# Kernel optimization log

Measured on AMD Instinct MI355X. Metric: run time of the kernel, lower is better.

Reference implementation:

```python
import math
import jax, jax.numpy as jnp
import numpy as np

H, D_H = 16, 128  # heads, head_dim; d = H*D_H = 2048

def _heads_view(w, rank):
    # w: (d, r) -> (H, r, d_h), matching torch view(H, d_h, r).transpose(1, 2)
    return jnp.transpose(w.reshape(H, D_H, rank), (0, 2, 1))

def setup_inputs() -> dict:
    key = jax.random.key(0)
    ks = jax.random.split(key, 9)
    d, rq, rk, rv = 2048, 512, 512, 512
    B, T = 2, 2048
    s = 0.02  # GPT-2 style init scale keeps logits numerically sane
    return {
        "x": jax.random.normal(ks[0], (B, T, d), dtype=jnp.float32),
        "q_down_w": jax.random.normal(ks[1], (rq, d), dtype=jnp.float32) * s,
        "k_down_w": jax.random.normal(ks[2], (rk, d), dtype=jnp.float32) * s,
        "v_down_w": jax.random.normal(ks[3], (rv, d), dtype=jnp.float32) * s,
        "q_up_w": jax.random.normal(ks[4], (d, rq), dtype=jnp.float32) * s,
        "k_up_w": jax.random.normal(ks[5], (d, rk), dtype=jnp.float32) * s,
        "v_up_w": jax.random.normal(ks[6], (d, rv), dtype=jnp.float32) * s,
        "out_w": jax.random.normal(ks[7], (d, d), dtype=jnp.float32) * s,
        "out_b": jnp.zeros((d,), dtype=jnp.float32),
    }

def reference(x, q_down_w, k_down_w, v_down_w, q_up_w, k_up_w, v_up_w, out_w, out_b):
    B, T, d = x.shape
    rq, rk, rv = q_down_w.shape[0], k_down_w.shape[0], v_down_w.shape[0]
    # Down projections (nn.Linear: x @ W^T)
    Qd = x @ q_down_w.T            # [B, T, rq]
    Kd = x @ k_down_w.T            # [B, S, rk] (S == T, no past_kv)
    Vd = x @ v_down_w.T            # [B, S, rv]
    S = Kd.shape[1]
    # Absorbed score matrix M: [H, rq, rk]
    Uq_h = _heads_view(q_up_w, rq)  # [H, rq, d_h]
    Uk_h = _heads_view(k_up_w, rk)  # [H, rk, d_h]
    M = jnp.einsum('hqd,hkd->hqk', Uq_h, Uk_h) * (1.0 / math.sqrt(D_H))
    # Logits via factorized path: [B,H,T,rk] then [B,H,T,S]
    Qm = jnp.einsum('btq,hqk->bhtk', Qd, M)
    logits = jnp.einsum('bhtk,bsk->bhts', Qm, Kd)
    # Causal mask (P = S - T = 0)
    P = S - T
    i = jnp.arange(T)[:, None]
    j = jnp.arange(S)[None, :]
    future = j > (P + i)
    logits = jnp.where(future[None, None], -jnp.inf, logits)
    attn = jax.nn.softmax(logits.astype(jnp.float32), axis=-1)
    attn = jnp.nan_to_num(attn).astype(x.dtype)
    # Values path
    Uv_h = _heads_view(v_up_w, rv)                      # [H, rv, d_h]
    V_up = jnp.einsum('bsr,hrd->bhsd', Vd, Uv_h)        # [B, H, S, d_h]
    ctx = jnp.einsum('bhts,bhsd->bhtd', attn, V_up)     # [B, H, T, d_h]
    ctx = jnp.transpose(ctx, (0, 2, 1, 3)).reshape(B, T, d)
    out = ctx @ out_w.T + out_b
    return out
```

## Files before the change

kernel.cpp:

```cpp
#include <hip/hip_runtime.h>
#include <stdint.h>

typedef __bf16 bf16x8 __attribute__((ext_vector_type(8)));
typedef float  f32x4  __attribute__((ext_vector_type(4)));
typedef unsigned short u16;
typedef u16 u16x8 __attribute__((ext_vector_type(8)));

__device__ __forceinline__ u16 f2bf(float f) {
  uint32_t u = __builtin_bit_cast(uint32_t, f);
  u += 0x7fffu + ((u >> 16) & 1u);
  return (u16)(u >> 16);
}

__device__ __forceinline__ void async_cp16(const void* src, void* lds) {
  __builtin_amdgcn_global_load_lds(
      (const __attribute__((address_space(1))) uint32_t*)src,
      (__attribute__((address_space(3))) uint32_t*)lds, 16, 0, 0);
}

struct CvtArgs {
  const float* in[8];
  u16* out[8];
  int n8[8];
  int nblk[8];
};
__global__ void cvt_multi(CvtArgs a) {
  int bx = blockIdx.x;
  int t = 0;
  while (t < 7 && bx >= a.nblk[t]) { bx -= a.nblk[t]; ++t; }
  const int i = bx * 256 + threadIdx.x;
  if (i >= a.n8[t]) return;
  const float4* p = (const float4*)a.in[t] + (size_t)i * 2;
  float4 va = p[0], vb = p[1];
  u16x8 r;
  r[0] = f2bf(va.x); r[1] = f2bf(va.y); r[2] = f2bf(va.z); r[3] = f2bf(va.w);
  r[4] = f2bf(vb.x); r[5] = f2bf(vb.y); r[6] = f2bf(vb.z); r[7] = f2bf(vb.w);
  ((u16x8*)a.out[t])[i] = r;
}

struct GemmB3 {
  const u16* A[3];
  const u16* Bm[3];
  u16* C[3];
  float alpha[3];
};

template<bool F32OUT>
__global__ __launch_bounds__(256, 2)
void gemm_bt(GemmB3 args, float* __restrict__ Cf, const float* __restrict__ bias,
             int M, int N, int K)
{
  __shared__ u16 At[128 * 32];
  __shared__ u16 Bt[128 * 32];
  const int z = blockIdx.z;
  const u16* __restrict__ A  = args.A[z];
  const u16* __restrict__ Bw = args.Bm[z];
  const int bm = blockIdx.x * 128;
  const int bn = blockIdx.y * 128;
  const int tid = threadIdx.x;
  const int w  = tid >> 6;
  const int l  = tid & 63;
  const int lr = l & 15;
  const int lg = l >> 4;
  const int wr = (w >> 1) * 64;
  const int wc = (w & 1) * 64;

  f32x4 acc[4][4];
  #pragma unroll
  for (int m = 0; m < 4; ++m) {
    #pragma unroll
    for (int n = 0; n < 4; ++n) acc[m][n] = (f32x4){0.f, 0.f, 0.f, 0.f};
  }

  for (int k0 = 0; k0 < K; k0 += 32) {
    __syncthreads();
    #pragma unroll
    for (int i = 0; i < 2; ++i) {
      const int gidx = i * 256 + tid;
      const int row  = gidx >> 2;
      const int g    = gidx & 3;
      const int gs   = (g - (row >> 1)) & 3;
      async_cp16(A  + (size_t)(bm + row) * K + k0 + gs * 8,
                 At + (size_t)(i * 256 + w * 64) * 8);
      async_cp16(Bw + (size_t)(bn + row) * K + k0 + gs * 8,
                 Bt + (size_t)(i * 256 + w * 64) * 8);
    }
    __syncthreads();
    bf16x8 af[4], bfr[4];
    #pragma unroll
    for (int m = 0; m < 4; ++m) {
      const int row = wr + m * 16 + lr;
      const int pos = (lg + (row >> 1)) & 3;
      af[m] = *(const bf16x8*)(At + row * 32 + pos * 8);
    }
    #pragma unroll
    for (int n = 0; n < 4; ++n) {
      const int row = wc + n * 16 + lr;
      const int pos = (lg + (row >> 1)) & 3;
      bfr[n] = *(const bf16x8*)(Bt + row * 32 + pos * 8);
    }
    #pragma unroll
    for (int m = 0; m < 4; ++m) {
      #pragma unroll
      for (int n = 0; n < 4; ++n)
        acc[m][n] = __builtin_amdgcn_mfma_f32_16x16x32_bf16(af[m], bfr[n], acc[m][n], 0, 0, 0);
    }
  }

  if constexpr (F32OUT) {
    #pragma unroll
    for (int n = 0; n < 4; ++n) {
      const int col = bn + wc + n * 16 + lr;
      const float bv = bias[col];
      #pragma unroll
      for (int m = 0; m < 4; ++m) {
        const int rbase = bm + wr + m * 16 + lg * 4;
        #pragma unroll
        for (int j = 0; j < 4; ++j)
          Cf[(size_t)(rbase + j) * N + col] = acc[m][n][j] + bv;
      }
    }
  } else {
    u16* __restrict__ C = args.C[z];
    const float alpha = args.alpha[z];
    #pragma unroll
    for (int n = 0; n < 4; ++n) {
      const int col = bn + wc + n * 16 + lr;
      #pragma unroll
      for (int m = 0; m < 4; ++m) {
        const int rbase = bm + wr + m * 16 + lg * 4;
        #pragma unroll
        for (int j = 0; j < 4; ++j)
          C[(size_t)(rbase + j) * N + col] = f2bf(acc[m][n][j] * alpha);
      }
    }
  }
}

__global__ __launch_bounds__(256, 2)
void mla_attn(const u16* __restrict__ Qu, const u16* __restrict__ Ku,
              const u16* __restrict__ Vtg, u16* __restrict__ ctx)
{
  __shared__ u16 Ktb[2][64 * 128];
  __shared__ u16 Vtb[2][128 * 64];
  __shared__ u16 Pb[4][16 * 72];

  const int bid = blockIdx.x;
  const int kk  = bid >> 5;
  const int qt  = (kk & 1) ? (kk >> 1) : (31 - (kk >> 1));
  const int bh  = bid & 31;
  const int b = bh >> 4, h = bh & 15;
  const int qbase = qt * 64;
  const int tid = threadIdx.x;
  const int w = tid >> 6, l = tid & 63, lr = l & 15, lg = l >> 4;
  const int T = 2048;
  const size_t rs = 2048;
  const u16* Qp = Qu + ((size_t)b * T) * rs + (size_t)h * 128;
  const u16* Kp = Ku + ((size_t)b * T) * rs + (size_t)h * 128;
  const u16* Vp = Vtg + (size_t)(h * 128) * 4096 + (size_t)b * T;

  bf16x8 qf[4];
  const int qrow = qbase + w * 16 + lr;
  #pragma unroll
  for (int f = 0; f < 4; ++f)
    qf[f] = *(const bf16x8*)(Qp + (size_t)qrow * rs + f * 32 + lg * 8);

  f32x4 acc[8];
  #pragma unroll
  for (int f = 0; f < 8; ++f) acc[f] = (f32x4){0.f, 0.f, 0.f, 0.f};
  f32x4 lacc = (f32x4){0.f, 0.f, 0.f, 0.f};
  float mrun[4];
  #pragma unroll
  for (int j = 0; j < 4; ++j) mrun[j] = -INFINITY;

  u16x8 onebits;
  #pragma unroll
  for (int e = 0; e < 8; ++e) onebits[e] = 0x3F80;
  const bf16x8 ones = __builtin_bit_cast(bf16x8, onebits);

  u16* Pw = Pb[w];
  const int nT = qt + 1;

  auto stage = [&](int buf, int it) {
    const int s0 = it * 64;
    #pragma unroll
    for (int i = 0; i < 4; ++i) {
      const int gidx = i * 256 + tid;
      const int s = gidx >> 4, g = gidx & 15;
      async_cp16(Kp + (size_t)(s0 + s) * rs + ((g ^ (s & 7)) * 8),
                 &Ktb[buf][(i * 256 + w * 64) * 8]);
    }
    #pragma unroll
    for (int i = 0; i < 4; ++i) {
      const int gidx = i * 256 + tid;
      const int dh = gidx >> 3, g = gidx & 7;
      async_cp16(Vp + (size_t)dh * 4096 + s0 + ((g ^ (dh & 7)) * 8),
                 &Vtb[buf][(i * 256 + w * 64) * 8]);
    }
  };

  stage(0, 0);
  int cur = 0;

  for (int it = 0; it < nT; ++it) {
    __syncthreads();
    if (it + 1 < nT) stage(cur ^ 1, it + 1);
    const u16* Kt = Ktb[cur];
    const u16* Vt = Vtb[cur];

    f32x4 c[4];
    #pragma unroll
    for (int ct = 0; ct < 4; ++ct) c[ct] = (f32x4){0.f, 0.f, 0.f, 0.f};
    __builtin_amdgcn_s_setprio(1);
    #pragma unroll
    for (int ct = 0; ct < 4; ++ct) {
      const int row = ct * 16 + lr;
      #pragma unroll
      for (int f = 0; f < 4; ++f) {
        bf16x8 kf = *(const bf16x8*)(Kt + row * 128 + (((f * 4 + lg) ^ (lr & 7)) * 8));
        c[ct] = __builtin_amdgcn_mfma_f32_16x16x32_bf16(qf[f], kf, c[ct], 0, 0, 0);
      }
    }
    __builtin_amdgcn_s_setprio(0);

    float p[4][4], mx[4];
    if (it == nT - 1) {
      const int qg = qbase + w * 16 + lg * 4;
      #pragma unroll
      for (int j = 0; j < 4; ++j) mx[j] = -INFINITY;
      #pragma unroll
      for (int ct = 0; ct < 4; ++ct) {
        const int s = it * 64 + ct * 16 + lr;
        #pragma unroll
        for (int j = 0; j < 4; ++j) {
          p[ct][j] = (s <= qg + j) ? c[ct][j] : -INFINITY;
          mx[j] = fmaxf(mx[j], p[ct][j]);
        }
      }
    } else {
      #pragma unroll
      for (int ct = 0; ct < 4; ++ct)
        #pragma unroll
        for (int j = 0; j < 4; ++j) p[ct][j] = c[ct][j];
      #pragma unroll
      for (int j = 0; j < 4; ++j)
        mx[j] = fmaxf(fmaxf(p[0][j], p[1][j]), fmaxf(p[2][j], p[3][j]));
    }
    #pragma unroll
    for (int j = 0; j < 4; ++j) {
      #pragma unroll
      for (int off = 1; off < 16; off <<= 1)
        mx[j] = fmaxf(mx[j], __shfl_xor(mx[j], off));
    }
    int over = 0;
    #pragma unroll
    for (int j = 0; j < 4; ++j) over |= (mx[j] > mrun[j] + 8.f) ? 1 : 0;
    if (__any(over)) {
      #pragma unroll
      for (int j = 0; j < 4; ++j) {
        const float mnew = fmaxf(mrun[j], mx[j]);
        const float scl = exp2f(mrun[j] - mnew);
        mrun[j] = mnew;
        lacc[j] *= scl;
        #pragma unroll
        for (int f = 0; f < 8; ++f) acc[f][j] *= scl;
      }
    }
    #pragma unroll
    for (int ct = 0; ct < 4; ++ct)
      #pragma unroll
      for (int j = 0; j < 4; ++j) p[ct][j] = exp2f(p[ct][j] - mrun[j]);

    #pragma unroll
    for (int ct = 0; ct < 4; ++ct)
      #pragma unroll
      for (int j = 0; j < 4; ++j)
        Pw[(lg * 4 + j) * 72 + ct * 16 + lr] = f2bf(p[ct][j]);
    asm volatile("s_waitcnt lgkmcnt(0)" ::: "memory");
    __builtin_amdgcn_sched_barrier(0);
    bf16x8 pf0 = *(const bf16x8*)(Pw + lr * 72 + lg * 8);
    bf16x8 pf1 = *(const bf16x8*)(Pw + lr * 72 + 32 + lg * 8);

    __builtin_amdgcn_s_setprio(1);
    lacc = __builtin_amdgcn_mfma_f32_16x16x32_bf16(pf0, ones, lacc, 0, 0, 0);
    lacc = __builtin_amdgcn_mfma_f32_16x16x32_bf16(pf1, ones, lacc, 0, 0, 0);
    #pragma unroll
    for (int f = 0; f < 8; ++f) {
      const int row = f * 16 + lr;
      bf16x8 v0 = *(const bf16x8*)(Vt + row * 64 + ((lg ^ (lr & 7)) * 8));
      bf16x8 v1 = *(const bf16x8*)(Vt + row * 64 + (((4 + lg) ^ (lr & 7)) * 8));
      acc[f] = __builtin_amdgcn_mfma_f32_16x16x32_bf16(pf0, v0, acc[f], 0, 0, 0);
      acc[f] = __builtin_amdgcn_mfma_f32_16x16x32_bf16(pf1, v1, acc[f], 0, 0, 0);
    }
    __builtin_amdgcn_s_setprio(0);
    cur ^= 1;
  }

  __syncthreads();
  u16* Ot = &Ktb[0][0];
  float inv[4];
  #pragma unroll
  for (int j = 0; j < 4; ++j) inv[j] = 1.f / lacc[j];
  #pragma unroll
  for (int f = 0; f < 8; ++f) {
    #pragma unroll
    for (int j = 0; j < 4; ++j) {
      const int q = w * 16 + lg * 4 + j;
      const int dh = f * 16 + lr;
      Ot[q * 128 + (dh ^ ((q & 7) << 3))] = f2bf(acc[f][j] * inv[j]);
    }
  }
  __syncthreads();
  const size_t obase = ((size_t)b * T + qbase) * rs + (size_t)h * 128;
  #pragma unroll
  for (int i = 0; i < 4; ++i) {
    const int gi = i * 256 + tid;
    const int q = gi >> 4, g = gi & 15;
    bf16x8 v = *(const bf16x8*)(Ot + q * 128 + ((g ^ (q & 7)) * 8));
    *(bf16x8*)(ctx + obase + (size_t)q * rs + g * 8) = v;
  }
}

extern "C" void kernel_launch(void* const* d_in, const int* in_sizes, int n_in,
                              void* d_out, int out_size, void* d_ws, size_t ws_size,
                              hipStream_t stream)
{
  (void)n_in; (void)out_size; (void)ws_size;
  const float* x   = (const float*)d_in[0];
  const float* qdw = (const float*)d_in[1];
  const float* kdw = (const float*)d_in[2];
  const float* vdw = (const float*)d_in[3];
  const float* quw = (const float*)d_in[4];
  const float* kuw = (const float*)d_in[5];
  const float* vuw = (const float*)d_in[6];
  const float* oww = (const float*)d_in[7];
  const float* ob  = (const float*)d_in[8];

  const int d = 2048, r = 512;
  const int BT = in_sizes[0] / d;

  u16* p = (u16*)d_ws;
  auto take = [&](size_t n) { u16* q = p; p += n; return q; };
  u16* xb  = take((size_t)BT * d);
  u16* wqd = take((size_t)r * d);
  u16* wkd = take((size_t)r * d);
  u16* wvd = take((size_t)r * d);
  u16* wqu = take((size_t)d * r);
  u16* wku = take((size_t)d * r);
  u16* wvu = take((size_t)d * r);
  u16* wow = take((size_t)d * d);
  u16* Qd  = take((size_t)BT * r);
  u16* Kd  = take((size_t)BT * r);
  u16* Vd  = take((size_t)BT * r);
  u16* Qu  = take((size_t)BT * d);
  u16* Ku  = take((size_t)BT * d);
  u16* Vtg = take((size_t)BT * d);
  u16* ctx = take((size_t)BT * d);

  CvtArgs ca;
  const float* ins[8] = {x, oww, qdw, kdw, vdw, quw, kuw, vuw};
  u16* outs[8]        = {xb, wow, wqd, wkd, wvd, wqu, wku, wvu};
  const size_t ns[8]  = {(size_t)BT * d, (size_t)d * d,
                         (size_t)r * d, (size_t)r * d, (size_t)r * d,
                         (size_t)d * r, (size_t)d * r, (size_t)d * r};
  int total_blk = 0;
  for (int t = 0; t < 8; ++t) {
    ca.in[t] = ins[t]; ca.out[t] = outs[t];
    ca.n8[t] = (int)(ns[t] / 8);
    ca.nblk[t] = (ca.n8[t] + 255) / 256;
    total_blk += ca.nblk[t];
  }
  cvt_multi<<<dim3(total_blk), dim3(256), 0, stream>>>(ca);

  GemmB3 g1;
  g1.A[0] = xb;  g1.A[1] = xb;  g1.A[2] = xb;
  g1.Bm[0] = wqd; g1.Bm[1] = wkd; g1.Bm[2] = wvd;
  g1.C[0] = Qd;  g1.C[1] = Kd;  g1.C[2] = Vd;
  g1.alpha[0] = 1.f; g1.alpha[1] = 1.f; g1.alpha[2] = 1.f;
  gemm_bt<false><<<dim3(BT / 128, r / 128, 3), dim3(256), 0, stream>>>(
      g1, nullptr, nullptr, BT, r, d);

  GemmB3 g2;
  g2.A[0] = Qd;  g2.A[1] = Kd;  g2.A[2] = Kd;
  g2.Bm[0] = wqu; g2.Bm[1] = wku; g2.Bm[2] = wku;
  g2.C[0] = Qu;  g2.C[1] = Ku;  g2.C[2] = Ku;
  g2.alpha[0] = 0.12751743f; g2.alpha[1] = 1.f; g2.alpha[2] = 1.f;
  gemm_bt<false><<<dim3(BT / 128, d / 128, 2), dim3(256), 0, stream>>>(
      g2, nullptr, nullptr, BT, d, r);

  GemmB3 g2v;
  g2v.A[0] = wvu; g2v.A[1] = wvu; g2v.A[2] = wvu;
  g2v.Bm[0] = Vd; g2v.Bm[1] = Vd; g2v.Bm[2] = Vd;
  g2v.C[0] = Vtg; g2v.C[1] = Vtg; g2v.C[2] = Vtg;
  g2v.alpha[0] = 1.f; g2v.alpha[1] = 1.f; g2v.alpha[2] = 1.f;
  gemm_bt<false><<<dim3(d / 128, BT / 128, 1), dim3(256), 0, stream>>>(
      g2v, nullptr, nullptr, d, BT, r);

  mla_attn<<<dim3(1024), dim3(256), 0, stream>>>(Qu, Ku, Vtg, ctx);

  GemmB3 g3;
  g3.A[0] = ctx; g3.A[1] = ctx; g3.A[2] = ctx;
  g3.Bm[0] = wow; g3.Bm[1] = wow; g3.Bm[2] = wow;
  g3.C[0] = nullptr; g3.C[1] = nullptr; g3.C[2] = nullptr;
  g3.alpha[0] = 1.f; g3.alpha[1] = 1.f; g3.alpha[2] = 1.f;
  gemm_bt<true><<<dim3(BT / 128, d / 128, 1), dim3(256), 0, stream>>>(
      g3, (float*)d_out, ob, BT, d, d);
}
```

Measured before the change: 242.5 us.

## Rewrite attention kernel with 32x32 MFMA, 128-row query tiles and register P exchange

The flash attention kernel now uses 32x32x16 bf16 MFMAs, computing S^T so each lane owns one query row. Each block covers 128 query rows (32 per wave) instead of 64, so half as many blocks are launched and each K/V tile staged in shared memory is reused by more queries. The P matrix is rebuilt for the PV MFMA through lane shuffles instead of a round trip through shared memory, and row sums are accumulated in registers instead of by an MFMA against a ones vector. Waves whose rows lie entirely before a K tile skip it under the causal mask. The costs are higher register pressure from the 16-wide accumulators, half as many blocks for load balancing, and a new swizzle whose correctness depends on matching index math.

```diff
diff --git a/kernel.cpp b/kernel.cpp
--- a/kernel.cpp
+++ b/kernel.cpp
@@ -3,13 +3,19 @@
 
 typedef __bf16 bf16x8 __attribute__((ext_vector_type(8)));
 typedef float  f32x4  __attribute__((ext_vector_type(4)));
+typedef float  f32x16 __attribute__((ext_vector_type(16)));
 typedef unsigned short u16;
+typedef unsigned int u32;
 typedef u16 u16x8 __attribute__((ext_vector_type(8)));
+typedef u32 u32x4 __attribute__((ext_vector_type(4)));
 
 __device__ __forceinline__ u16 f2bf(float f) {
   uint32_t u = __builtin_bit_cast(uint32_t, f);
   u += 0x7fffu + ((u >> 16) & 1u);
   return (u16)(u >> 16);
+}
+__device__ __forceinline__ u32 pack2(float lo, float hi) {
+  return (u32)f2bf(lo) | ((u32)f2bf(hi) << 16);
 }
 
 __device__ __forceinline__ void async_cp16(const void* src, void* lds) {
@@ -67,10 +73,9 @@
 
   f32x4 acc[4][4];
   #pragma unroll
-  for (int m = 0; m < 4; ++m) {
+  for (int m = 0; m < 4; ++m)
     #pragma unroll
     for (int n = 0; n < 4; ++n) acc[m][n] = (f32x4){0.f, 0.f, 0.f, 0.f};
-  }
 
   for (int k0 = 0; k0 < K; k0 += 32) {
     __syncthreads();
@@ -100,11 +105,10 @@
       bfr[n] = *(const bf16x8*)(Bt + row * 32 + pos * 8);
     }
     #pragma unroll
-    for (int m = 0; m < 4; ++m) {
+    for (int m = 0; m < 4; ++m)
       #pragma unroll
       for (int n = 0; n < 4; ++n)
         acc[m][n] = __builtin_amdgcn_mfma_f32_16x16x32_bf16(af[m], bfr[n], acc[m][n], 0, 0, 0);
-    }
   }
 
   if constexpr (F32OUT) {
@@ -143,60 +147,55 @@
 {
   __shared__ u16 Ktb[2][64 * 128];
   __shared__ u16 Vtb[2][128 * 64];
-  __shared__ u16 Pb[4][16 * 72];
 
   const int bid = blockIdx.x;
   const int kk  = bid >> 5;
-  const int qt  = (kk & 1) ? (kk >> 1) : (31 - (kk >> 1));
+  const int qt  = (kk & 1) ? (kk >> 1) : (15 - (kk >> 1));
   const int bh  = bid & 31;
   const int b = bh >> 4, h = bh & 15;
-  const int qbase = qt * 64;
+  const int qbase = qt * 128;
   const int tid = threadIdx.x;
-  const int w = tid >> 6, l = tid & 63, lr = l & 15, lg = l >> 4;
+  const int w = tid >> 6, l = tid & 63;
+  const int ql = l & 31;
+  const int hi = l >> 5;
+  const bool hb = (hi != 0);
   const int T = 2048;
   const size_t rs = 2048;
+
   const u16* Qp = Qu + ((size_t)b * T) * rs + (size_t)h * 128;
   const u16* Kp = Ku + ((size_t)b * T) * rs + (size_t)h * 128;
   const u16* Vp = Vtg + (size_t)(h * 128) * 4096 + (size_t)b * T;
 
-  bf16x8 qf[4];
-  const int qrow = qbase + w * 16 + lr;
-  #pragma unroll
-  for (int f = 0; f < 4; ++f)
-    qf[f] = *(const bf16x8*)(Qp + (size_t)qrow * rs + f * 32 + lg * 8);
-
-  f32x4 acc[8];
-  #pragma unroll
-  for (int f = 0; f < 8; ++f) acc[f] = (f32x4){0.f, 0.f, 0.f, 0.f};
-  f32x4 lacc = (f32x4){0.f, 0.f, 0.f, 0.f};
-  float mrun[4];
-  #pragma unroll
-  for (int j = 0; j < 4; ++j) mrun[j] = -INFINITY;
-
-  u16x8 onebits;
-  #pragma unroll
-  for (int e = 0; e < 8; ++e) onebits[e] = 0x3F80;
-  const bf16x8 ones = __builtin_bit_cast(bf16x8, onebits);
-
-  u16* Pw = Pb[w];
-  const int nT = qt + 1;
+  const int qw = qbase + w * 32;
+  const int qg = qw + ql;
+
+  bf16x8 qf[8];
+  #pragma unroll
+  for (int kb = 0; kb < 8; ++kb)
+    qf[kb] = *(const bf16x8*)(Qp + (size_t)qg * rs + kb * 16 + hi * 8);
+
+  f32x16 acc[4];
+  #pragma unroll
+  for (int dt = 0; dt < 4; ++dt)
+    #pragma unroll
+    for (int r = 0; r < 16; ++r) acc[dt][r] = 0.f;
+  float mrun = -1.0e30f, lsum = 0.f;
+
+  const int ksr = tid >> 4;
+  const u16* kb0 = Kp + (size_t)ksr * rs + (((tid & 15) ^ (ksr & 15)) * 8);
+  const int vsr = tid >> 3;
+  const u16* vb0 = Vp + (size_t)vsr * 4096 + (((tid & 7) ^ (vsr & 7)) * 8);
+
+  const int nT = 2 * qt + 2;
 
   auto stage = [&](int buf, int it) {
     const int s0 = it * 64;
     #pragma unroll
-    for (int i = 0; i < 4; ++i) {
-      const int gidx = i * 256 + tid;
-      const int s = gidx >> 4, g = gidx & 15;
-      async_cp16(Kp + (size_t)(s0 + s) * rs + ((g ^ (s & 7)) * 8),
-                 &Ktb[buf][(i * 256 + w * 64) * 8]);
-    }
-    #pragma unroll
-    for (int i = 0; i < 4; ++i) {
-      const int gidx = i * 256 + tid;
-      const int dh = gidx >> 3, g = gidx & 7;
-      async_cp16(Vp + (size_t)dh * 4096 + s0 + ((g ^ (dh & 7)) * 8),
-                 &Vtb[buf][(i * 256 + w * 64) * 8]);
-    }
+    for (int i = 0; i < 4; ++i)
+      async_cp16(kb0 + (size_t)(s0 + i * 16) * rs, &Ktb[buf][(i * 256 + w * 64) * 8]);
+    #pragma unroll
+    for (int i = 0; i < 4; ++i)
+      async_cp16(vb0 + (size_t)(i * 32) * 4096 + s0, &Vtb[buf][(i * 256 + w * 64) * 8]);
   };
 
   stage(0, 0);
@@ -205,119 +204,110 @@
   for (int it = 0; it < nT; ++it) {
     __syncthreads();
     if (it + 1 < nT) stage(cur ^ 1, it + 1);
-    const u16* Kt = Ktb[cur];
-    const u16* Vt = Vtb[cur];
-
-    f32x4 c[4];
-    #pragma unroll
-    for (int ct = 0; ct < 4; ++ct) c[ct] = (f32x4){0.f, 0.f, 0.f, 0.f};
-    __builtin_amdgcn_s_setprio(1);
-    #pragma unroll
-    for (int ct = 0; ct < 4; ++ct) {
-      const int row = ct * 16 + lr;
+    const int s0 = it * 64;
+    if (s0 <= qw + 31) {
+      const u16* Kt = Ktb[cur];
+      const u16* Vt = Vtb[cur];
+      const bool diag = (it == (qw >> 6));
       #pragma unroll
-      for (int f = 0; f < 4; ++f) {
-        bf16x8 kf = *(const bf16x8*)(Kt + row * 128 + (((f * 4 + lg) ^ (lr & 7)) * 8));
-        c[ct] = __builtin_amdgcn_mfma_f32_16x16x32_bf16(qf[f], kf, c[ct], 0, 0, 0);
+      for (int st = 0; st < 2; ++st) {
+        f32x16 c;
+        #pragma unroll
+        for (int r = 0; r < 16; ++r) c[r] = 0.f;
+        __builtin_amdgcn_s_setprio(1);
+        #pragma unroll
+        for (int kb = 0; kb < 8; ++kb) {
+          bf16x8 kf = *(const bf16x8*)(Kt + (st * 32 + ql) * 128 +
+                                       (((2 * kb + hi) ^ (ql & 15)) * 8));
+          c = __builtin_amdgcn_mfma_f32_32x32x16_bf16(kf, qf[kb], c, 0, 0, 0);
+        }
+        __builtin_amdgcn_s_setprio(0);
+
+        float p[16];
+        if (diag) {
+          #pragma unroll
+          for (int r = 0; r < 16; ++r) {
+            const int sgl = s0 + st * 32 + 4 * hi + (r & 3) + 8 * (r >> 2);
+            p[r] = (sgl <= qg) ? c[r] : -INFINITY;
+          }
+        } else {
+          #pragma unroll
+          for (int r = 0; r < 16; ++r) p[r] = c[r];
+        }
+        float mx = p[0];
+        #pragma unroll
+        for (int r = 1; r < 16; ++r) mx = fmaxf(mx, p[r]);
+        mx = fmaxf(mx, __shfl_xor(mx, 32));
+        if (__any(mx > mrun + 8.f)) {
+          const float mnew = fmaxf(mrun, mx);
+          const float scl = exp2f(mrun - mnew);
+          mrun = mnew;
+          lsum *= scl;
+          #pragma unroll
+          for (int dt = 0; dt < 4; ++dt)
+            #pragma unroll
+            for (int r = 0; r < 16; ++r) acc[dt][r] *= scl;
+        }
+        float psum = 0.f;
+        #pragma unroll
+        for (int r = 0; r < 16; ++r) { p[r] = exp2f(p[r] - mrun); psum += p[r]; }
+        lsum += psum + __shfl_xor(psum, 32);
+
+        u32 P0 = pack2(p[0], p[1]),   P1 = pack2(p[2], p[3]);
+        u32 P2 = pack2(p[4], p[5]),   P3 = pack2(p[6], p[7]);
+        u32 P4 = pack2(p[8], p[9]),   P5 = pack2(p[10], p[11]);
+        u32 P6 = pack2(p[12], p[13]), P7 = pack2(p[14], p[15]);
+        u32 X0 = __shfl_xor(P0, 32), X1 = __shfl_xor(P1, 32);
+        u32 X2 = __shfl_xor(P2, 32), X3 = __shfl_xor(P3, 32);
+        u32 X4 = __shfl_xor(P4, 32), X5 = __shfl_xor(P5, 32);
+        u32 X6 = __shfl_xor(P6, 32), X7 = __shfl_xor(P7, 32);
+        const bf16x8 f0 = __builtin_bit_cast(bf16x8,
+            (u32x4){hb ? X2 : P0, hb ? X3 : P1, hb ? P2 : X0, hb ? P3 : X1});
+        const bf16x8 f1 = __builtin_bit_cast(bf16x8,
+            (u32x4){hb ? X6 : P4, hb ? X7 : P5, hb ? P6 : X4, hb ? P7 : X5});
+
+        __builtin_amdgcn_s_setprio(1);
+        #pragma unroll
+        for (int dt = 0; dt < 4; ++dt) {
+          const int vrow = (dt * 32 + ql) * 64;
+          bf16x8 v0 = *(const bf16x8*)(Vt + vrow + (((2 * (2 * st)     + hi) ^ (ql & 7)) * 8));
+          bf16x8 v1 = *(const bf16x8*)(Vt + vrow + (((2 * (2 * st + 1) + hi) ^ (ql & 7)) * 8));
+          acc[dt] = __builtin_amdgcn_mfma_f32_32x32x16_bf16(v0, f0, acc[dt], 0, 0, 0);
+          acc[dt] = __builtin_amdgcn_mfma_f32_32x32x16_bf16(v1, f1, acc[dt], 0, 0, 0);
+        }
+        __builtin_amdgcn_s_setprio(0);
       }
     }
-    __builtin_amdgcn_s_setprio(0);
-
-    float p[4][4], mx[4];
-    if (it == nT - 1) {
-      const int qg = qbase + w * 16 + lg * 4;
-      #pragma unroll
-      for (int j = 0; j < 4; ++j) mx[j] = -INFINITY;
-      #pragma unroll
-      for (int ct = 0; ct < 4; ++ct) {
-        const int s = it * 64 + ct * 16 + lr;
-        #pragma unroll
-        for (int j = 0; j < 4; ++j) {
-          p[ct][j] = (s <= qg + j) ? c[ct][j] : -INFINITY;
-          mx[j] = fmaxf(mx[j], p[ct][j]);
-        }
-      }
-    } else {
-      #pragma unroll
-      for (int ct = 0; ct < 4; ++ct)
-        #pragma unroll
-        for (int j = 0; j < 4; ++j) p[ct][j] = c[ct][j];
-      #pragma unroll
-      for (int j = 0; j < 4; ++j)
-        mx[j] = fmaxf(fmaxf(p[0][j], p[1][j]), fmaxf(p[2][j], p[3][j]));
-    }
-    #pragma unroll
-    for (int j = 0; j < 4; ++j) {
-      #pragma unroll
-      for (int off = 1; off < 16; off <<= 1)
-        mx[j] = fmaxf(mx[j], __shfl_xor(mx[j], off));
-    }
-    int over = 0;
-    #pragma unroll
-    for (int j = 0; j < 4; ++j) over |= (mx[j] > mrun[j] + 8.f) ? 1 : 0;
-    if (__any(over)) {
-      #pragma unroll
-      for (int j = 0; j < 4; ++j) {
-        const float mnew = fmaxf(mrun[j], mx[j]);
-        const float scl = exp2f(mrun[j] - mnew);
-        mrun[j] = mnew;
-        lacc[j] *= scl;
-        #pragma unroll
-        for (int f = 0; f < 8; ++f) acc[f][j] *= scl;
-      }
-    }
-    #pragma unroll
-    for (int ct = 0; ct < 4; ++ct)
-      #pragma unroll
-      for (int j = 0; j < 4; ++j) p[ct][j] = exp2f(p[ct][j] - mrun[j]);
-
-    #pragma unroll
-    for (int ct = 0; ct < 4; ++ct)
-      #pragma unroll
-      for (int j = 0; j < 4; ++j)
-        Pw[(lg * 4 + j) * 72 + ct * 16 + lr] = f2bf(p[ct][j]);
-    asm volatile("s_waitcnt lgkmcnt(0)" ::: "memory");
-    __builtin_amdgcn_sched_barrier(0);
-    bf16x8 pf0 = *(const bf16x8*)(Pw + lr * 72 + lg * 8);
-    bf16x8 pf1 = *(const bf16x8*)(Pw + lr * 72 + 32 + lg * 8);
-
-    __builtin_amdgcn_s_setprio(1);
-    lacc = __builtin_amdgcn_mfma_f32_16x16x32_bf16(pf0, ones, lacc, 0, 0, 0);
-    lacc = __builtin_amdgcn_mfma_f32_16x16x32_bf16(pf1, ones, lacc, 0, 0, 0);
-    #pragma unroll
-    for (int f = 0; f < 8; ++f) {
-      const int row = f * 16 + lr;
-      bf16x8 v0 = *(const bf16x8*)(Vt + row * 64 + ((lg ^ (lr & 7)) * 8));
-      bf16x8 v1 = *(const bf16x8*)(Vt + row * 64 + (((4 + lg) ^ (lr & 7)) * 8));
-      acc[f] = __builtin_amdgcn_mfma_f32_16x16x32_bf16(pf0, v0, acc[f], 0, 0, 0);
-      acc[f] = __builtin_amdgcn_mfma_f32_16x16x32_bf16(pf1, v1, acc[f], 0, 0, 0);
-    }
-    __builtin_amdgcn_s_setprio(0);
     cur ^= 1;
   }
 
   __syncthreads();
   u16* Ot = &Ktb[0][0];
-  float inv[4];
-  #pragma unroll
-  for (int j = 0; j < 4; ++j) inv[j] = 1.f / lacc[j];
-  #pragma unroll
-  for (int f = 0; f < 8; ++f) {
-    #pragma unroll
-    for (int j = 0; j < 4; ++j) {
-      const int q = w * 16 + lg * 4 + j;
-      const int dh = f * 16 + lr;
-      Ot[q * 128 + (dh ^ ((q & 7) << 3))] = f2bf(acc[f][j] * inv[j]);
+  const float inv = 1.f / lsum;
+  const int orow = w * 32 + ql;
+  #pragma unroll
+  for (int dt = 0; dt < 4; ++dt) {
+    #pragma unroll
+    for (int rq = 0; rq < 4; ++rq) {
+      const int dhb = dt * 32 + 8 * rq + 4 * hi;
+      const int dhs = dhb ^ ((ql & 15) << 3);
+      u16 e0 = f2bf(acc[dt][rq * 4 + 0] * inv);
+      u16 e1 = f2bf(acc[dt][rq * 4 + 1] * inv);
+      u16 e2 = f2bf(acc[dt][rq * 4 + 2] * inv);
+      u16 e3 = f2bf(acc[dt][rq * 4 + 3] * inv);
+      u32 w0 = (u32)e0 | ((u32)e1 << 16);
+      u32 w1 = (u32)e2 | ((u32)e3 << 16);
+      *(u32*)(Ot + orow * 128 + dhs)     = w0;
+      *(u32*)(Ot + orow * 128 + dhs + 2) = w1;
     }
   }
   __syncthreads();
-  const size_t obase = ((size_t)b * T + qbase) * rs + (size_t)h * 128;
-  #pragma unroll
-  for (int i = 0; i < 4; ++i) {
-    const int gi = i * 256 + tid;
-    const int q = gi >> 4, g = gi & 15;
-    bf16x8 v = *(const bf16x8*)(Ot + q * 128 + ((g ^ (q & 7)) * 8));
-    *(bf16x8*)(ctx + obase + (size_t)q * rs + g * 8) = v;
+  #pragma unroll
+  for (int i = 0; i < 8; ++i) {
+    const int n = i * 256 + tid;
+    const int q = n >> 4, g = n & 15;
+    bf16x8 v = *(const bf16x8*)(Ot + q * 128 + ((g ^ (q & 15)) * 8));
+    *(bf16x8*)(ctx + ((size_t)b * T + qbase + q) * rs + h * 128 + g * 8) = v;
   }
 }
 
@@ -396,7 +386,7 @@
   gemm_bt<false><<<dim3(d / 128, BT / 128, 1), dim3(256), 0, stream>>>(
       g2v, nullptr, nullptr, d, BT, r);
 
-  mla_attn<<<dim3(1024), dim3(256), 0, stream>>>(Qu, Ku, Vtg, ctx);
+  mla_attn<<<dim3(512), dim3(256), 0, stream>>>(Qu, Ku, Vtg, ctx);
 
   GemmB3 g3;
   g3.A[0] = ctx; g3.A[1] = ctx; g3.A[2] = ctx;
```

After: 239.1 us. About the same (-1.4%).
